# Performance work log

Measured on AMD Instinct MI355X. Metric: run time of the kernel, lower is better.

Reference implementation:

```python
import jax, jax.numpy as jnp
import numpy as np

N_NODES = 50000
N_EDGES = 800000
NEG_SLOPE = 0.2  # GATConv default
BN_EPS = 1e-5


def _seg_softmax(logits, seg, n):
    # per-target-node softmax over incoming edges (PyG softmax w/ +1e-16)
    m = jax.ops.segment_max(logits, seg, num_segments=n)
    m = jnp.where(jnp.isfinite(m), m, 0.0)
    e = jnp.exp(logits - m[seg])
    s = jax.ops.segment_sum(e, seg, num_segments=n)
    return e / (s[seg] + 1e-16)


def _gat_conv(x, src, dst, W, a_src, a_dst, b, concat):
    # x: [N, Fin]; W: [Fin, H*C]; a_src/a_dst: [H, C]
    n = x.shape[0]
    H, C = a_src.shape
    h = (x @ W).reshape(n, H, C)
    al_s = jnp.einsum('nhc,hc->nh', h, a_src)
    al_d = jnp.einsum('nhc,hc->nh', h, a_dst)
    logits = jax.nn.leaky_relu(al_s[src] + al_d[dst], NEG_SLOPE)  # [E, H]
    alpha = _seg_softmax(logits, dst, n)                           # [E, H]
    out = jax.ops.segment_sum(h[src] * alpha[:, :, None], dst, num_segments=n)
    out = out.reshape(n, H * C) if concat else out.mean(axis=1)
    return out + b


def _bn(x, g, b):
    mu = jnp.mean(x, axis=0)
    var = jnp.mean((x - mu) ** 2, axis=0)
    return (x - mu) * jax.lax.rsqrt(var + BN_EPS) * g + b


def _gat_params(key, fin, heads, ch, scale=0.1):
    k1, k2, k3 = jax.random.split(key, 3)
    W = jax.random.normal(k1, (fin, heads * ch), jnp.float32) * scale
    a_s = jax.random.normal(k2, (heads, ch), jnp.float32) * scale
    a_d = jax.random.normal(k3, (heads, ch), jnp.float32) * scale
    return W, a_s, a_d


def setup_inputs() -> dict:
    key = jax.random.key(0)
    ks = jax.random.split(key, 12)
    inp = {}
    inp['x'] = jax.random.normal(ks[0], (N_NODES, 3), jnp.float32)
    inp['edge_index'] = jax.random.randint(ks[1], (2, N_EDGES), 0, N_NODES, jnp.int64 if jax.config.jax_enable_x64 else jnp.int32)
    inp['W11'], inp['as11'], inp['ad11'] = _gat_params(ks[2], 3, 8, 8)
    inp['b11'] = jnp.zeros((64,), jnp.float32)
    inp['W12'], inp['as12'], inp['ad12'] = _gat_params(ks[3], 64, 8, 8)
    inp['b12'] = jnp.zeros((64,), jnp.float32)
    inp['g1'] = jnp.ones((64,), jnp.float32)
    inp['be1'] = jnp.zeros((64,), jnp.float32)
    inp['W21'], inp['as21'], inp['ad21'] = _gat_params(ks[4], 64, 8, 32)
    inp['b21'] = jnp.zeros((256,), jnp.float32)
    inp['W22'], inp['as22'], inp['ad22'] = _gat_params(ks[5], 256, 8, 32)
    inp['b22'] = jnp.zeros((256,), jnp.float32)
    inp['g2'] = jnp.ones((256,), jnp.float32)
    inp['be2'] = jnp.zeros((256,), jnp.float32)
    inp['W31'], inp['as31'], inp['ad31'] = _gat_params(ks[6], 256, 8, 64)
    inp['b31'] = jnp.zeros((512,), jnp.float32)
    inp['W32'], inp['as32'], inp['ad32'] = _gat_params(ks[7], 512, 8, 1)
    inp['b32'] = jnp.zeros((1,), jnp.float32)
    return inp


def reference(x, edge_index,
              W11, as11, ad11, b11, W12, as12, ad12, b12, g1, be1,
              W21, as21, ad21, b21, W22, as22, ad22, b22, g2, be2,
              W31, as31, ad31, b31, W32, as32, ad32, b32):
    n = x.shape[0]
    loops = jnp.arange(n, dtype=edge_index.dtype)
    src = jnp.concatenate([edge_index[0], loops])  # add_self_loops=True
    dst = jnp.concatenate([edge_index[1], loops])
    # GAT(3, 64, 2): conv -> relu -> conv
    h = jax.nn.relu(_gat_conv(x, src, dst, W11, as11, ad11, b11, True))
    h = _gat_conv(h, src, dst, W12, as12, ad12, b12, True)
    h = jax.nn.leaky_relu(_bn(h, g1, be1), 0.1)
    # GAT(64, 256, 2)
    h = jax.nn.relu(_gat_conv(h, src, dst, W21, as21, ad21, b21, True))
    h = _gat_conv(h, src, dst, W22, as22, ad22, b22, True)
    h = jax.nn.leaky_relu(_bn(h, g2, be2), 0.1)
    # GAT(256, 512, 2, 1): conv -> relu -> conv(concat=False)
    h = jax.nn.relu(_gat_conv(h, src, dst, W31, as31, ad31, b31, True))
    h = _gat_conv(h, src, dst, W32, as32, ad32, b32, False)
    return jax.nn.sigmoid(h)
```

## Files before the change

### kernel.cpp

```cpp
#include <hip/hip_runtime.h>
#include <math.h>

typedef short short8 __attribute__((ext_vector_type(8)));
typedef short short4v __attribute__((ext_vector_type(4)));
typedef float f32x4 __attribute__((ext_vector_type(4)));

__device__ __forceinline__ unsigned short f2bf(float v){
  unsigned u = __builtin_bit_cast(unsigned, v);
  u += 0x7FFFu + ((u >> 16) & 1u);
  return (unsigned short)(u >> 16);
}
__device__ __forceinline__ float bf2f(unsigned short b){
  unsigned u = ((unsigned)b) << 16;
  return __builtin_bit_cast(float, u);
}

__global__ void k_deg_prep(const int* __restrict__ dstv, int* __restrict__ deg, int E,
                           const float* __restrict__ W11, const float* __restrict__ W12,
                           const float* __restrict__ W21, const float* __restrict__ W22,
                           const float* __restrict__ W31,
                           unsigned short* __restrict__ bh, unsigned short* __restrict__ bl){
  int i = blockIdx.x*blockDim.x + threadIdx.x;
  if (i < E) atomicAdd(&deg[dstv[i]], 1);
  if (i < 221184){
    const float* W; int K, kpsh, off, Nn;
    if (i < 4096)       { W=W11; K=3;   kpsh=6; off=0;     Nn=64;  }
    else if (i < 8192)  { W=W12; K=64;  kpsh=6; off=4096;  Nn=64;  }
    else if (i < 24576) { W=W21; K=64;  kpsh=6; off=8192;  Nn=256; }
    else if (i < 90112) { W=W22; K=256; kpsh=8; off=24576; Nn=256; }
    else                { W=W31; K=256; kpsh=8; off=90112; Nn=512; }
    int j = i - off;
    int Kp = 1 << kpsh;
    int n = j >> kpsh, k = j & (Kp-1);
    float v = (k < K) ? W[(size_t)k*Nn + n] : 0.0f;
    unsigned short h = f2bf(v);
    bh[i] = h;
    bl[i] = f2bf(v - bf2f(h));
  }
}

__global__ __launch_bounds__(1024)
void k_scan1(const int* __restrict__ deg, int* __restrict__ off,
             int* __restrict__ bsum, int N){
  __shared__ int wpre[16];
  int tid = threadIdx.x;
  int lane = tid & 63, wv = tid >> 6;
  int i = blockIdx.x*1024 + tid;
  int v = (i < N) ? deg[i] : 0;
  int incl = v;
  #pragma unroll
  for (int d = 1; d < 64; d <<= 1){
    int t = __shfl_up(incl, d, 64);
    if (lane >= d) incl += t;
  }
  if (lane == 63) wpre[wv] = incl;
  __syncthreads();
  if (tid < 16){
    int x = wpre[tid];
    int ix = x;
    #pragma unroll
    for (int d = 1; d < 16; d <<= 1){
      int t = __shfl_up(ix, d, 16);
      if (tid >= d) ix += t;
    }
    wpre[tid] = ix - x;
    if (tid == 15) bsum[blockIdx.x] = ix;
  }
  __syncthreads();
  if (i < N) off[i+1] = wpre[wv] + incl;
}

__global__ void k_scan2(int* __restrict__ bsum, int* __restrict__ bpre, int nb){
  int t = threadIdx.x;
  int v = (t < nb) ? bsum[t] : 0;
  int incl = v;
  #pragma unroll
  for (int d = 1; d < 64; d <<= 1){
    int u = __shfl_up(incl, d, 64);
    if (t >= d) incl += u;
  }
  if (t < nb) bpre[t] = incl - v;
}

__global__ __launch_bounds__(1024)
void k_scan3(const int* __restrict__ deg, int* __restrict__ off,
             const int* __restrict__ bpre, int* __restrict__ cursor, int N){
  int i = blockIdx.x*1024 + threadIdx.x;
  if (i < N){
    int base = bpre[blockIdx.x];
    int incl = off[i+1] + base;
    off[i+1] = incl;
    cursor[i] = incl - deg[i];
    if (i == 0) off[0] = 0;
  }
}

__global__ void k_fill(const int* __restrict__ srcv, const int* __restrict__ dstv,
                       int* __restrict__ cursor, int* __restrict__ csr, int E){
  int e = blockIdx.x*blockDim.x + threadIdx.x;
  if (e < E){
    int d = dstv[e];
    int p = atomicAdd(&cursor[d], 1);
    csr[p] = srcv[e];
  }
}

__global__ __launch_bounds__(256)
void k_bn_stats(const unsigned short* __restrict__ x, float* __restrict__ psum,
                float* __restrict__ psq, int N, int HC){
  int f   = threadIdx.x & (HC-1);
  int sub = threadIdx.x / HC;
  int subs = 256 / HC;
  int slot = blockIdx.x*subs + sub;
  int stride = gridDim.x*subs;
  float s = 0.f, q = 0.f;
  for (int r = slot; r < N; r += stride){
    float v = bf2f(x[(size_t)r*HC + f]);
    s += v; q += v*v;
  }
  psum[(size_t)slot*HC + f] = s;
  psq [(size_t)slot*HC + f] = q;
}

__global__ __launch_bounds__(256)
void k_bn_coef(const float* __restrict__ psum, const float* __restrict__ psq,
               const float* __restrict__ g, const float* __restrict__ b,
               float* __restrict__ sc, float* __restrict__ sh,
               float invN, int HC, int nb){
  int f = blockIdx.x;
  int t = threadIdx.x;
  float s = 0.f, q = 0.f;
  for (int r = t; r < nb; r += 256){
    s += psum[(size_t)r*HC + f];
    q += psq [(size_t)r*HC + f];
  }
  #pragma unroll
  for (int d = 1; d < 64; d <<= 1){
    s += __shfl_xor(s, d, 64);
    q += __shfl_xor(q, d, 64);
  }
  __shared__ float ss[4], qq[4];
  int wv = t >> 6, ln = t & 63;
  if (ln == 0){ ss[wv] = s; qq[wv] = q; }
  __syncthreads();
  if (t == 0){
    s = ss[0]+ss[1]+ss[2]+ss[3];
    q = qq[0]+qq[1]+qq[2]+qq[3];
    float mu  = s*invN;
    float var = q*invN - mu*mu;
    float rs  = rsqrtf(var + 1e-5f) * g[f];
    sc[f] = rs;
    sh[f] = b[f] - mu*rs;
  }
}

template<int BN, int AFMT>
__global__ __launch_bounds__((BN==64)?256:512)
void gemm_mfma(const void* __restrict__ Av, const unsigned short* __restrict__ Bh,
               const unsigned short* __restrict__ Bl,
               const float* __restrict__ bnsc, const float* __restrict__ bnsh,
               const float* __restrict__ a_s, const float* __restrict__ a_d,
               unsigned short* __restrict__ Pb, float* __restrict__ Ds,
               float* __restrict__ Dd, int M, int K){
  constexpr int WAVES   = (BN==64) ? 4 : 8;
  constexpr int BLOCK   = WAVES*64;
  constexpr int WAVES_N = BN/64;
  constexpr int WAVES_M = WAVES/WAVES_N;
  constexpr int WM      = 64/WAVES_M;
  constexpr int MF      = WM/16;
  constexpr int CH      = (BN==512)?64 : (BN==256)?32 : 8;
  constexpr int TERMS   = (AFMT==0) ? 3 : 2;
  const int Kp = (K + 63) & ~(int)63;

  __shared__ char lds[(TERMS==3)?16384:8192];

  int tid  = threadIdx.x;
  int lane = tid & 63;
  int wid  = tid >> 6;
  int wn = wid % WAVES_N;
  int wm = wid / WAVES_N;
  int n0w = wn*64;
  int wm0 = wm*WM;
  int m0 = blockIdx.x * 64;

  f32x4 acc[MF][4];
  #pragma unroll
  for (int i = 0; i < MF; ++i)
    #pragma unroll
    for (int j = 0; j < 4; ++j)
      acc[i][j] = (f32x4){0.f,0.f,0.f,0.f};

  constexpr int SITER = 512/BLOCK;

  for (int k0 = 0; k0 < Kp; k0 += 64){
    __syncthreads();
    #pragma unroll
    for (int it = 0; it < SITER; ++it){
      int i = it*BLOCK + tid;
      int row = i >> 3, c8 = i & 7;
      int gm = m0 + row;
      int gk = k0 + c8*8;
      int off = row*128 + ((c8 ^ (row&7))<<4);
      if constexpr (AFMT == 2){
        short8 hv = {0,0,0,0,0,0,0,0};
        if (gm < M) hv = *(const short8*)((const unsigned short*)Av + (size_t)gm*K + gk);
        *(short8*)(lds + off) = hv;
      } else if constexpr (AFMT == 1){
        short8 raw = {0,0,0,0,0,0,0,0};
        if (gm < M) raw = *(const short8*)((const unsigned short*)Av + (size_t)gm*K + gk);
        short8 hi;
        #pragma unroll
        for (int j=0;j<8;++j){
          float u = bf2f((unsigned short)raw[j])*bnsc[gk+j] + bnsh[gk+j];
          u = u > 0.f ? u : 0.1f*u;
          if (gm >= M) u = 0.f;
          hi[j] = (short)f2bf(u);
        }
        *(short8*)(lds + off) = hi;
      } else {
        const float* A = (const float*)Av;
        float v[8];
        if (gm < M && gk + 8 <= K){
          const float* ap = A + (size_t)gm*K + gk;
          float4 x0 = *(const float4*)ap;
          float4 x1 = *(const float4*)(ap+4);
          v[0]=x0.x; v[1]=x0.y; v[2]=x0.z; v[3]=x0.w;
          v[4]=x1.x; v[5]=x1.y; v[6]=x1.z; v[7]=x1.w;
        } else {
          #pragma unroll
          for (int j=0;j<8;++j){
            int gkj = gk + j;
            v[j] = (gm < M && gkj < K) ? A[(size_t)gm*K + gkj] : 0.0f;
          }
        }
        short8 hi, lo;
        #pragma unroll
        for (int j=0;j<8;++j){
          unsigned short hb = f2bf(v[j]);
          hi[j] = (short)hb;
          lo[j] = (short)f2bf(v[j] - bf2f(hb));
        }
        *(short8*)(lds + off) = hi;
        *(short8*)(lds + 8192 + off) = lo;
      }
    }
    __syncthreads();
    #pragma unroll
    for (int kk = 0; kk < 2; ++kk){
      short8 bhf[4], blf[4];
      #pragma unroll
      for (int nf = 0; nf < 4; ++nf){
        int ncol = n0w + nf*16 + (lane & 15);
        int kidx = k0 + kk*32 + ((lane>>4)<<3);
        size_t bo = (size_t)ncol*Kp + kidx;
        bhf[nf] = *(const short8*)(Bh + bo);
        blf[nf] = *(const short8*)(Bl + bo);
      }
      #pragma unroll
      for (int mt = 0; mt < MF; ++mt){
        int row = wm0 + mt*16 + (lane & 15);
        int c8 = kk*4 + (lane>>4);
        int off = row*128 + ((c8 ^ (row&7))<<4);
        short8 ah = *(const short8*)(lds + off);
        #pragma unroll
        for (int nf = 0; nf < 4; ++nf){
          acc[mt][nf] = __builtin_amdgcn_mfma_f32_16x16x32_bf16(ah, bhf[nf], acc[mt][nf], 0,0,0);
          acc[mt][nf] = __builtin_amdgcn_mfma_f32_16x16x32_bf16(ah, blf[nf], acc[mt][nf], 0,0,0);
        }
        if constexpr (TERMS == 3){
          short8 al = *(const short8*)(lds + 8192 + off);
          #pragma unroll
          for (int nf = 0; nf < 4; ++nf)
            acc[mt][nf] = __builtin_amdgcn_mfma_f32_16x16x32_bf16(al, bhf[nf], acc[mt][nf], 0,0,0);
        }
      }
    }
  }

  float asv[4], adv[4];
  #pragma unroll
  for (int nf=0; nf<4; ++nf){
    int gcol = n0w + nf*16 + (lane&15);
    asv[nf] = a_s[gcol];
    adv[nf] = a_d[gcol];
  }
  #pragma unroll
  for (int mt = 0; mt < MF; ++mt){
    #pragma unroll
    for (int r = 0; r < 4; ++r){
      int gm = m0 + wm0 + mt*16 + ((lane>>4)<<2) + r;
      bool ok = gm < M;
      #pragma unroll
      for (int nf=0;nf<4;++nf){
        if (ok) Pb[(size_t)gm*BN + n0w + nf*16 + (lane&15)] = f2bf(acc[mt][nf][r]);
      }
      if constexpr (CH == 64){
        float ps = acc[mt][0][r]*asv[0] + acc[mt][1][r]*asv[1]
                 + acc[mt][2][r]*asv[2] + acc[mt][3][r]*asv[3];
        float pd = acc[mt][0][r]*adv[0] + acc[mt][1][r]*adv[1]
                 + acc[mt][2][r]*adv[2] + acc[mt][3][r]*adv[3];
        #pragma unroll
        for (int d2=1; d2<16; d2<<=1){ ps += __shfl_xor(ps,d2,64); pd += __shfl_xor(pd,d2,64); }
        if (ok && (lane&15)==0){
          int head = n0w >> 6;
          Ds[(size_t)gm*8 + head] = ps;
          Dd[(size_t)gm*8 + head] = pd;
        }
      } else if constexpr (CH == 32){
        float ps0 = acc[mt][0][r]*asv[0] + acc[mt][1][r]*asv[1];
        float ps1 = acc[mt][2][r]*asv[2] + acc[mt][3][r]*asv[3];
        float pd0 = acc[mt][0][r]*adv[0] + acc[mt][1][r]*adv[1];
        float pd1 = acc[mt][2][r]*adv[2] + acc[mt][3][r]*adv[3];
        #pragma unroll
        for (int d2=1; d2<16; d2<<=1){
          ps0 += __shfl_xor(ps0,d2,64); ps1 += __shfl_xor(ps1,d2,64);
          pd0 += __shfl_xor(pd0,d2,64); pd1 += __shfl_xor(pd1,d2,64);
        }
        if (ok && (lane&15)==0){
          int head = n0w >> 5;
          Ds[(size_t)gm*8 + head]     = ps0;
          Ds[(size_t)gm*8 + head + 1] = ps1;
          Dd[(size_t)gm*8 + head]     = pd0;
          Dd[(size_t)gm*8 + head + 1] = pd1;
        }
      } else {
        #pragma unroll
        for (int nf=0;nf<4;++nf){
          float ps = acc[mt][nf][r]*asv[nf];
          float pd = acc[mt][nf][r]*adv[nf];
          #pragma unroll
          for (int d2=1; d2<8; d2<<=1){ ps += __shfl_xor(ps,d2,64); pd += __shfl_xor(pd,d2,64); }
          if (ok && (lane&7)==0){
            int head = nf*2 + ((lane>>3)&1);
            Ds[(size_t)gm*8 + head] = ps;
            Dd[(size_t)gm*8 + head] = pd;
          }
        }
      }
    }
  }
}

template<int HC, int ACT>
__global__ __launch_bounds__(256)
void k_agg(const unsigned short* __restrict__ Pb, const float* __restrict__ Ds,
           const float* __restrict__ Dd, const int* __restrict__ off,
           const int* __restrict__ csr, const float* __restrict__ bias,
           unsigned short* __restrict__ outb, int N){
  __shared__ float salpha[4][512];
  int lane = threadIdx.x & 63;
  int wid  = threadIdx.x >> 6;
  int n = blockIdx.x*4 + wid;
  if (n >= N) return;
  int o0 = off[n], deg = off[n+1]-o0;

  float aldn[8];
  {
    const float* dn = Dd + (unsigned)n*8u;
    float4 x0 = *(const float4*)dn;
    float4 x1 = *(const float4*)(dn+4);
    aldn[0]=x0.x; aldn[1]=x0.y; aldn[2]=x0.z; aldn[3]=x0.w;
    aldn[4]=x1.x; aldn[5]=x1.y; aldn[6]=x1.z; aldn[7]=x1.w;
  }

  if (deg < 64){
    int nE = deg + 1;
    int myidx = (lane < deg) ? csr[o0+lane] : n;
    bool active = (lane < nE);
    float v[8];
    {
      const float* dp = Ds + (unsigned)myidx*8u;
      float4 x0 = *(const float4*)dp;
      float4 x1 = *(const float4*)(dp+4);
      float t[8] = {x0.x,x0.y,x0.z,x0.w,x1.x,x1.y,x1.z,x1.w};
      #pragma unroll
      for (int h=0;h<8;++h){
        float u = t[h] + aldn[h];
        u = u > 0.f ? u : 0.2f*u;
        v[h] = active ? u : -1e30f;
      }
    }
    float m[8];
    #pragma unroll
    for (int h=0;h<8;++h) m[h]=v[h];
    #pragma unroll
    for (int d=1; d<64; d<<=1)
      #pragma unroll
      for (int h=0;h<8;++h) m[h] = fmaxf(m[h], __shfl_xor(m[h], d, 64));
    float sv[8], s[8];
    #pragma unroll
    for (int h=0;h<8;++h){ sv[h] = active ? __expf(v[h]-m[h]) : 0.f; s[h]=sv[h]; }
    #pragma unroll
    for (int d=1; d<64; d<<=1)
      #pragma unroll
      for (int h=0;h<8;++h) s[h] += __shfl_xor(s[h], d, 64);
    if (active){
      #pragma unroll
      for (int h=0;h<8;++h) salpha[wid][lane*8+h] = sv[h] / (s[h] + 1e-16f);
    }
    asm volatile("s_waitcnt lgkmcnt(0)" ::: "memory");

    if constexpr (HC == 512){
      int myh = lane >> 3;
      float acc[8] = {0,0,0,0,0,0,0,0};
      const unsigned short* Pl = Pb + lane*8;
      for (int e=0; e<nE; ++e){
        int src = __shfl(myidx, e, 64);
        float alpha = salpha[wid][e*8 + myh];
        short8 w = *(const short8*)(Pl + (unsigned)src*512u);
        #pragma unroll
        for (int j=0;j<8;++j) acc[j] += alpha * bf2f((unsigned short)w[j]);
      }
      #pragma unroll
      for (int j=0;j<8;++j){
        int f = lane*8 + j;
        float u = acc[j] + bias[f];
        if (ACT == 1) u = fmaxf(u, 0.0f);
        outb[(unsigned)n*512u + f] = f2bf(u);
      }
    } else if constexpr (HC == 256){
      int sub = lane >> 5, fl = lane & 31;
      int h = fl >> 2;
      float acc[8] = {0,0,0,0,0,0,0,0};
      const unsigned short* Pl = Pb + fl*8;
      for (int e=0; e<nE; e+=2){
        int eg = e + sub;
        bool val = eg < nE;
        int src = __shfl(myidx, val ? eg : 0, 64);
        float alpha = val ? salpha[wid][eg*8 + h] : 0.f;
        short8 w = *(const short8*)(Pl + (unsigned)src*256u);
        #pragma unroll
        for (int j=0;j<8;++j) acc[j] += alpha * bf2f((unsigned short)w[j]);
      }
      #pragma unroll
      for (int j=0;j<8;++j) acc[j] += __shfl_xor(acc[j], 32, 64);
      if (sub == 0){
        short8 ov;
        #pragma unroll
        for (int j=0;j<8;++j){
          int f = fl*8 + j;
          float u = acc[j] + bias[f];
          if (ACT == 1) u = fmaxf(u, 0.0f);
          ov[j] = (short)f2bf(u);
        }
        *(short8*)(outb + (unsigned)n*256u + fl*8) = ov;
      }
    } else {
      int sub = lane >> 3, fl = lane & 7;
      float acc[8] = {0,0,0,0,0,0,0,0};
      const unsigned short* Pl = Pb + fl*8;
      for (int e=0; e<nE; e+=8){
        int eg = e + sub;
        bool val = eg < nE;
        int src = __shfl(myidx, val ? eg : 0, 64);
        float alpha = val ? salpha[wid][eg*8 + fl] : 0.f;
        short8 w = *(const short8*)(Pl + (unsigned)src*64u);
        #pragma unroll
        for (int j=0;j<8;++j) acc[j] += alpha * bf2f((unsigned short)w[j]);
      }
      #pragma unroll
      for (int j=0;j<8;++j){
        acc[j] += __shfl_xor(acc[j], 8, 64);
        acc[j] += __shfl_xor(acc[j], 16, 64);
        acc[j] += __shfl_xor(acc[j], 32, 64);
      }
      if (sub == 0){
        short8 ov;
        #pragma unroll
        for (int j=0;j<8;++j){
          int f = fl*8 + j;
          float u = acc[j] + bias[f];
          if (ACT == 1) u = fmaxf(u, 0.0f);
          ov[j] = (short)f2bf(u);
        }
        *(short8*)(outb + (unsigned)n*64u + fl*8) = ov;
      }
    }
  } else {
    constexpr int R = HC/64;
    int myh = lane >> 3;
    float m[8];
    #pragma unroll
    for (int h=0;h<8;++h) m[h] = -1e30f;
    for (int e = lane; e <= deg; e += 64){
      int src = (e < deg) ? csr[o0+e] : n;
      const float* ap = Ds + (size_t)src*8;
      #pragma unroll
      for (int h=0;h<8;++h){
        float u = ap[h] + aldn[h];
        u = u > 0.f ? u : 0.2f*u;
        m[h] = fmaxf(m[h], u);
      }
    }
    #pragma unroll
    for (int d=1; d<64; d<<=1)
      #pragma unroll
      for (int h=0;h<8;++h) m[h] = fmaxf(m[h], __shfl_xor(m[h], d, 64));
    float s[8] = {0,0,0,0,0,0,0,0};
    for (int e = lane; e <= deg; e += 64){
      int src = (e < deg) ? csr[o0+e] : n;
      const float* ap = Ds + (size_t)src*8;
      #pragma unroll
      for (int h=0;h<8;++h){
        float u = ap[h] + aldn[h];
        u = u > 0.f ? u : 0.2f*u;
        s[h] += __expf(u - m[h]);
      }
    }
    #pragma unroll
    for (int d=1; d<64; d<<=1)
      #pragma unroll
      for (int h=0;h<8;++h) s[h] += __shfl_xor(s[h], d, 64);
    float mh = m[myh];
    float rsh = 1.0f/(s[myh] + 1e-16f);
    float adh = aldn[myh];
    float acc[R];
    #pragma unroll
    for (int j=0;j<R;++j) acc[j]=0.f;
    for (int e = 0; e <= deg; ++e){
      int src = (e < deg) ? csr[o0+e] : n;
      float u = Ds[(size_t)src*8 + myh] + adh;
      u = u > 0.f ? u : 0.2f*u;
      float alpha = __expf(u - mh) * rsh;
      const unsigned short* hp = Pb + (size_t)src*HC + lane*R;
      if constexpr (R == 1){
        acc[0] += alpha * bf2f(hp[0]);
      } else if constexpr (R == 4){
        short4v w = *(const short4v*)hp;
        #pragma unroll
        for (int j=0;j<4;++j) acc[j] += alpha * bf2f((unsigned short)w[j]);
      } else {
        short8 w = *(const short8*)hp;
        #pragma unroll
        for (int j=0;j<8;++j) acc[j] += alpha * bf2f((unsigned short)w[j]);
      }
    }
    #pragma unroll
    for (int j = 0; j < R; ++j){
      int f = lane*R + j;
      float u = acc[j] + bias[f];
      if (ACT == 1) u = fmaxf(u, 0.0f);
      outb[(size_t)n*HC + f] = f2bf(u);
    }
  }
}

__global__ __launch_bounds__(256)
void gemm8(const unsigned short* __restrict__ Qb, const float* __restrict__ W,
           float* __restrict__ h8, int M){
  int lane = threadIdx.x & 63;
  int gw = (blockIdx.x*blockDim.x + threadIdx.x) >> 6;
  int nw = (gridDim.x*blockDim.x) >> 6;
  float w[8][8];
  const float* wp = W + lane*64;
  #pragma unroll
  for (int j=0;j<8;++j){
    float4 a = *(const float4*)(wp + j*8);
    float4 b = *(const float4*)(wp + j*8 + 4);
    w[j][0]=a.x; w[j][1]=a.y; w[j][2]=a.z; w[j][3]=a.w;
    w[j][4]=b.x; w[j][5]=b.y; w[j][6]=b.z; w[j][7]=b.w;
  }
  for (int n = gw; n < M; n += nw){
    short8 v8 = *(const short8*)(Qb + (size_t)n*512 + lane*8);
    float p[8] = {0,0,0,0,0,0,0,0};
    #pragma unroll
    for (int j=0;j<8;++j){
      float x = bf2f((unsigned short)v8[j]);
      #pragma unroll
      for (int o=0;o<8;++o) p[o] += x * w[j][o];
    }
    #pragma unroll
    for (int d=1; d<64; d<<=1)
      #pragma unroll
      for (int o=0;o<8;++o) p[o] += __shfl_xor(p[o], d, 64);
    if (lane == 0){
      float4 y0 = make_float4(p[0],p[1],p[2],p[3]);
      float4 y1 = make_float4(p[4],p[5],p[6],p[7]);
      *(float4*)(h8 + (size_t)n*8)     = y0;
      *(float4*)(h8 + (size_t)n*8 + 4) = y1;
    }
  }
}

__global__ __launch_bounds__(256)
void k_final(const float* __restrict__ h8, const float* __restrict__ a_s,
             const float* __restrict__ a_d, const int* __restrict__ off,
             const int* __restrict__ csr, const float* __restrict__ b32,
             float* __restrict__ outp, int N){
  int lane = threadIdx.x & 63;
  int wv   = threadIdx.x >> 6;
  int n = blockIdx.x*4 + wv;
  if (n >= N) return;
  int o0 = off[n], deg = off[n+1]-o0;
  float asv[8], adv[8];
  #pragma unroll
  for (int h=0;h<8;++h){ asv[h]=a_s[h]; adv[h]=a_d[h]; }
  float aldn[8];
  {
    const float* hp = h8 + (size_t)n*8;
    float4 x0 = *(const float4*)hp;
    float4 x1 = *(const float4*)(hp+4);
    float hn[8] = {x0.x,x0.y,x0.z,x0.w,x1.x,x1.y,x1.z,x1.w};
    #pragma unroll
    for (int h=0;h<8;++h) aldn[h] = hn[h]*adv[h];
  }

  if (deg < 64){
    int nE = deg + 1;
    int src = (lane < deg) ? csr[o0+lane] : n;
    bool act = (lane < nE);
    float hs[8];
    {
      const float* hp = h8 + (size_t)src*8;
      float4 x0 = *(const float4*)hp;
      float4 x1 = *(const float4*)(hp+4);
      hs[0]=x0.x; hs[1]=x0.y; hs[2]=x0.z; hs[3]=x0.w;
      hs[4]=x1.x; hs[5]=x1.y; hs[6]=x1.z; hs[7]=x1.w;
    }
    float v[8];
    #pragma unroll
    for (int h=0;h<8;++h){
      float u = hs[h]*asv[h] + aldn[h];
      u = u > 0.f ? u : 0.2f*u;
      v[h] = act ? u : -1e30f;
    }
    float m[8];
    #pragma unroll
    for (int h=0;h<8;++h) m[h]=v[h];
    #pragma unroll
    for (int d=1; d<64; d<<=1)
      #pragma unroll
      for (int h=0;h<8;++h) m[h] = fmaxf(m[h], __shfl_xor(m[h], d, 64));
    float s[8], t[8];
    #pragma unroll
    for (int h=0;h<8;++h){
      float e = act ? __expf(v[h]-m[h]) : 0.f;
      s[h]=e; t[h]=e*hs[h];
    }
    #pragma unroll
    for (int d=1; d<64; d<<=1)
      #pragma unroll
      for (int h=0;h<8;++h){
        s[h] += __shfl_xor(s[h], d, 64);
        t[h] += __shfl_xor(t[h], d, 64);
      }
    if (lane == 0){
      float o = 0.f;
      #pragma unroll
      for (int h=0;h<8;++h) o += t[h]/(s[h]+1e-16f);
      o = o*0.125f + b32[0];
      outp[n] = 1.0f/(1.0f + __expf(-o));
    }
  } else if (lane == 0){
    float m[8], s[8], agg[8];
    #pragma unroll
    for (int h=0;h<8;++h){ m[h]=-1e30f; s[h]=0.f; agg[h]=0.f; }
    for (int e = 0; e <= deg; ++e){
      int src = (e < deg) ? csr[o0+e] : n;
      #pragma unroll
      for (int h=0;h<8;++h){
        float u = h8[(size_t)src*8+h]*asv[h] + aldn[h];
        u = u > 0.f ? u : 0.2f*u;
        m[h] = fmaxf(m[h], u);
      }
    }
    for (int e = 0; e <= deg; ++e){
      int src = (e < deg) ? csr[o0+e] : n;
      #pragma unroll
      for (int h=0;h<8;++h){
        float u = h8[(size_t)src*8+h]*asv[h] + aldn[h];
        u = u > 0.f ? u : 0.2f*u;
        float ex = __expf(u - m[h]);
        s[h] += ex;
        agg[h] += ex * h8[(size_t)src*8+h];
      }
    }
    float o = 0.f;
    #pragma unroll
    for (int h=0;h<8;++h) o += agg[h]/(s[h]+1e-16f);
    o = o*0.125f + b32[0];
    outp[n] = 1.0f/(1.0f + __expf(-o));
  }
}

extern "C" void kernel_launch(void* const* d_in, const int* in_sizes, int n_in,
                              void* d_out, int out_size, void* d_ws, size_t ws_size,
                              hipStream_t stream){
  int N = in_sizes[0]/3;
  int E = in_sizes[1]/2;
  const float* x    = (const float*)d_in[0];
  const int*   ei   = (const int*)  d_in[1];
  const float* W11  = (const float*)d_in[2];
  const float* as11 = (const float*)d_in[3];
  const float* ad11 = (const float*)d_in[4];
  const float* b11  = (const float*)d_in[5];
  const float* W12  = (const float*)d_in[6];
  const float* as12 = (const float*)d_in[7];
  const float* ad12 = (const float*)d_in[8];
  const float* b12  = (const float*)d_in[9];
  const float* g1   = (const float*)d_in[10];
  const float* be1  = (const float*)d_in[11];
  const float* W21  = (const float*)d_in[12];
  const float* as21 = (const float*)d_in[13];
  const float* ad21 = (const float*)d_in[14];
  const float* b21  = (const float*)d_in[15];
  const float* W22  = (const float*)d_in[16];
  const float* as22 = (const float*)d_in[17];
  const float* ad22 = (const float*)d_in[18];
  const float* b22  = (const float*)d_in[19];
  const float* g2   = (const float*)d_in[20];
  const float* be2  = (const float*)d_in[21];
  const float* W31  = (const float*)d_in[22];
  const float* as31 = (const float*)d_in[23];
  const float* ad31 = (const float*)d_in[24];
  const float* b31  = (const float*)d_in[25];
  const float* W32  = (const float*)d_in[26];
  const float* as32 = (const float*)d_in[27];
  const float* ad32 = (const float*)d_in[28];
  const float* b32  = (const float*)d_in[29];

  char* ws = (char*)d_ws;
  size_t o = 0;
  auto alloc = [&](size_t bytes)->char*{
    char* p = ws + o;
    o = (o + bytes + 255) & ~(size_t)255;
    return p;
  };
  int*   deg    = (int*)  alloc((size_t)N*4);
  int*   off    = (int*)  alloc((size_t)(N+1)*4);
  int*   cursor = (int*)  alloc((size_t)N*4);
  int*   csr    = (int*)  alloc((size_t)E*4);
  int*   bsum   = (int*)  alloc(64*4);
  int*   bpre   = (int*)  alloc(64*4);
  unsigned short* bh = (unsigned short*)alloc(221184*2);
  unsigned short* bl = (unsigned short*)alloc(221184*2);
  float* h8     = (float*)alloc((size_t)N*8*4);
  float* psum   = (float*)alloc(1024*64*4);
  float* psq    = (float*)alloc(1024*64*4);
  float* bnsc   = (float*)alloc(1024);
  float* bnsh   = (float*)alloc(1024);
  unsigned short* Pb = (unsigned short*)alloc((size_t)N*512*2);
  unsigned short* Qb = (unsigned short*)alloc((size_t)N*512*2);
  float* Dsb    = (float*)alloc((size_t)N*8*4);
  float* Ddb    = (float*)alloc((size_t)N*8*4);
  (void)ws_size;

  const int BT11=0, BT12=4096, BT21=8192, BT22=24576, BT31=90112;

  hipMemsetAsync(deg, 0, (size_t)N*4, stream);
  int eb = (E+255)/256;
  int nb1k = (N+1023)/1024;
  k_deg_prep<<<eb, 256, 0, stream>>>(ei+E, deg, E, W11, W12, W21, W22, W31, bh, bl);
  k_scan1<<<nb1k, 1024, 0, stream>>>(deg, off, bsum, N);
  k_scan2<<<1, 64, 0, stream>>>(bsum, bpre, nb1k);
  k_scan3<<<nb1k, 1024, 0, stream>>>(deg, off, bpre, cursor, N);
  k_fill<<<eb, 256, 0, stream>>>(ei, ei+E, cursor, csr, E);

  int mb = (N+63)/64;
  int nb4 = (N+3)/4;
  float invN = 1.0f/(float)N;

  gemm_mfma<64,0><<<mb, 256, 0, stream>>>(x, bh+BT11, bl+BT11, nullptr, nullptr,
                                          as11, ad11, Pb, Dsb, Ddb, N, 3);
  k_agg<64,1><<<nb4, 256, 0, stream>>>(Pb, Dsb, Ddb, off, csr, b11, Qb, N);

  gemm_mfma<64,2><<<mb, 256, 0, stream>>>(Qb, bh+BT12, bl+BT12, nullptr, nullptr,
                                          as12, ad12, Pb, Dsb, Ddb, N, 64);
  k_agg<64,0><<<nb4, 256, 0, stream>>>(Pb, Dsb, Ddb, off, csr, b12, Qb, N);
  k_bn_stats<<<256, 256, 0, stream>>>(Qb, psum, psq, N, 64);
  k_bn_coef<<<64, 256, 0, stream>>>(psum, psq, g1, be1, bnsc, bnsh, invN, 64, 1024);

  gemm_mfma<256,1><<<mb, 512, 0, stream>>>(Qb, bh+BT21, bl+BT21, bnsc, bnsh,
                                           as21, ad21, Pb, Dsb, Ddb, N, 64);
  k_agg<256,1><<<nb4, 256, 0, stream>>>(Pb, Dsb, Ddb, off, csr, b21, Qb, N);

  gemm_mfma<256,2><<<mb, 512, 0, stream>>>(Qb, bh+BT22, bl+BT22, nullptr, nullptr,
                                           as22, ad22, Pb, Dsb, Ddb, N, 256);
  k_agg<256,0><<<nb4, 256, 0, stream>>>(Pb, Dsb, Ddb, off, csr, b22, Qb, N);
  k_bn_stats<<<256, 256, 0, stream>>>(Qb, psum, psq, N, 256);
  k_bn_coef<<<256, 256, 0, stream>>>(psum, psq, g2, be2, bnsc, bnsh, invN, 256, 256);

  gemm_mfma<512,1><<<mb, 512, 0, stream>>>(Qb, bh+BT31, bl+BT31, bnsc, bnsh,
                                           as31, ad31, Pb, Dsb, Ddb, N, 256);
  k_agg<512,1><<<nb4, 256, 0, stream>>>(Pb, Dsb, Ddb, off, csr, b31, Qb, N);

  gemm8<<<1024, 256, 0, stream>>>(Qb, W32, h8, N);
  k_final<<<nb4, 256, 0, stream>>>(h8, as32, ad32, off, csr, b32,
                                   (float*)d_out, N);
}
```

Before: 1.031 ms.

## Fuse batchnorm statistics and final 512x8 projection into aggregation kernels

The aggregation kernel gains a MODE template parameter. MODE 1 accumulates per-feature sum and sum-of-squares in shared memory with atomics and writes per-block partials, which removes the separate k_bn_stats pass that re-read the bf16 activations. MODE 2 multiplies each aggregated row by W32 held in shared memory and writes the 8-wide projection directly, which drops gemm8 and the 512-wide bf16 write and read of the last layer. In exchange, shared-memory atomic contention rises, and k_bn_coef now reduces over 12500 partial blocks instead of 256 or 1024.

After: 1.226 ms. 1.19x slower.

```diff
diff --git a/kernel.cpp b/kernel.cpp
--- a/kernel.cpp
+++ b/kernel.cpp
@@ -106,23 +106,6 @@
 }
 
 __global__ __launch_bounds__(256)
-void k_bn_stats(const unsigned short* __restrict__ x, float* __restrict__ psum,
-                float* __restrict__ psq, int N, int HC){
-  int f   = threadIdx.x & (HC-1);
-  int sub = threadIdx.x / HC;
-  int subs = 256 / HC;
-  int slot = blockIdx.x*subs + sub;
-  int stride = gridDim.x*subs;
-  float s = 0.f, q = 0.f;
-  for (int r = slot; r < N; r += stride){
-    float v = bf2f(x[(size_t)r*HC + f]);
-    s += v; q += v*v;
-  }
-  psum[(size_t)slot*HC + f] = s;
-  psq [(size_t)slot*HC + f] = q;
-}
-
-__global__ __launch_bounds__(256)
 void k_bn_coef(const float* __restrict__ psum, const float* __restrict__ psq,
                const float* __restrict__ g, const float* __restrict__ b,
                float* __restrict__ sc, float* __restrict__ sh,
@@ -341,243 +324,277 @@
   }
 }
 
-template<int HC, int ACT>
+template<int HC, int ACT, int MODE>
 __global__ __launch_bounds__(256)
 void k_agg(const unsigned short* __restrict__ Pb, const float* __restrict__ Ds,
            const float* __restrict__ Dd, const int* __restrict__ off,
            const int* __restrict__ csr, const float* __restrict__ bias,
-           unsigned short* __restrict__ outb, int N){
+           unsigned short* __restrict__ outb, float* __restrict__ x1,
+           float* __restrict__ x2, const float* __restrict__ W32, int N){
   __shared__ float salpha[4][512];
-  int lane = threadIdx.x & 63;
-  int wid  = threadIdx.x >> 6;
+  __shared__ float sstat[(MODE==1)? 2*HC : 1];
+  __shared__ float ws32[(MODE==2)? 4096 : 1];
+  int tid  = threadIdx.x;
+  int lane = tid & 63;
+  int wid  = tid >> 6;
+
+  if constexpr (MODE == 1){
+    if (tid < HC){ sstat[tid] = 0.f; sstat[HC+tid] = 0.f; }
+    __syncthreads();
+  }
+  if constexpr (MODE == 2){
+    #pragma unroll
+    for (int i = 0; i < 4; ++i){
+      float4 w4 = *(const float4*)(W32 + i*1024 + tid*4);
+      *(float4*)(ws32 + i*1024 + tid*4) = w4;
+    }
+    __syncthreads();
+  }
+
   int n = blockIdx.x*4 + wid;
-  if (n >= N) return;
-  int o0 = off[n], deg = off[n+1]-o0;
-
-  float aldn[8];
-  {
-    const float* dn = Dd + (unsigned)n*8u;
-    float4 x0 = *(const float4*)dn;
-    float4 x1 = *(const float4*)(dn+4);
-    aldn[0]=x0.x; aldn[1]=x0.y; aldn[2]=x0.z; aldn[3]=x0.w;
-    aldn[4]=x1.x; aldn[5]=x1.y; aldn[6]=x1.z; aldn[7]=x1.w;
-  }
-
-  if (deg < 64){
-    int nE = deg + 1;
-    int myidx = (lane < deg) ? csr[o0+lane] : n;
-    bool active = (lane < nE);
-    float v[8];
+  bool vn = (n < N);
+  float p8[8];
+  #pragma unroll
+  for (int o=0;o<8;++o) p8[o] = 0.f;
+
+  if (vn){
+    int o0 = off[n], deg = off[n+1]-o0;
+
+    float aldn[8];
     {
-      const float* dp = Ds + (unsigned)myidx*8u;
-      float4 x0 = *(const float4*)dp;
-      float4 x1 = *(const float4*)(dp+4);
-      float t[8] = {x0.x,x0.y,x0.z,x0.w,x1.x,x1.y,x1.z,x1.w};
-      #pragma unroll
-      for (int h=0;h<8;++h){
-        float u = t[h] + aldn[h];
+      const float* dn = Dd + (unsigned)n*8u;
+      float4 x0v = *(const float4*)dn;
+      float4 x1v = *(const float4*)(dn+4);
+      aldn[0]=x0v.x; aldn[1]=x0v.y; aldn[2]=x0v.z; aldn[3]=x0v.w;
+      aldn[4]=x1v.x; aldn[5]=x1v.y; aldn[6]=x1v.z; aldn[7]=x1v.w;
+    }
+
+    if (deg < 64){
+      int nE = deg + 1;
+      int myidx = (lane < deg) ? csr[o0+lane] : n;
+      bool active = (lane < nE);
+      float v[8];
+      {
+        const float* dp = Ds + (unsigned)myidx*8u;
+        float4 x0v = *(const float4*)dp;
+        float4 x1v = *(const float4*)(dp+4);
+        float t[8] = {x0v.x,x0v.y,x0v.z,x0v.w,x1v.x,x1v.y,x1v.z,x1v.w};
+        #pragma unroll
+        for (int h=0;h<8;++h){
+          float u = t[h] + aldn[h];
+          u = u > 0.f ? u : 0.2f*u;
+          v[h] = active ? u : -1e30f;
+        }
+      }
+      float m[8];
+      #pragma unroll
+      for (int h=0;h<8;++h) m[h]=v[h];
+      #pragma unroll
+      for (int d=1; d<64; d<<=1)
+        #pragma unroll
+        for (int h=0;h<8;++h) m[h] = fmaxf(m[h], __shfl_xor(m[h], d, 64));
+      float sv[8], s[8];
+      #pragma unroll
+      for (int h=0;h<8;++h){ sv[h] = active ? __expf(v[h]-m[h]) : 0.f; s[h]=sv[h]; }
+      #pragma unroll
+      for (int d=1; d<64; d<<=1)
+        #pragma unroll
+        for (int h=0;h<8;++h) s[h] += __shfl_xor(s[h], d, 64);
+      if (active){
+        #pragma unroll
+        for (int h=0;h<8;++h) salpha[wid][lane*8+h] = sv[h] / (s[h] + 1e-16f);
+      }
+      asm volatile("s_waitcnt lgkmcnt(0)" ::: "memory");
+
+      if constexpr (HC == 512){
+        int myh = lane >> 3;
+        float acc[8] = {0,0,0,0,0,0,0,0};
+        const unsigned short* Pl = Pb + lane*8;
+        for (int e=0; e<nE; ++e){
+          int src = __shfl(myidx, e, 64);
+          float alpha = salpha[wid][e*8 + myh];
+          short8 w = *(const short8*)(Pl + (unsigned)src*512u);
+          #pragma unroll
+          for (int j=0;j<8;++j) acc[j] += alpha * bf2f((unsigned short)w[j]);
+        }
+        #pragma unroll
+        for (int j=0;j<8;++j){
+          int f = lane*8 + j;
+          float u = acc[j] + bias[f];
+          if (ACT == 1) u = fmaxf(u, 0.0f);
+          if constexpr (MODE == 2){
+            #pragma unroll
+            for (int o=0;o<8;++o) p8[o] += u * ws32[f*8+o];
+          } else {
+            outb[(unsigned)n*512u + f] = f2bf(u);
+            if constexpr (MODE == 1){
+              atomicAdd(&sstat[f], u);
+              atomicAdd(&sstat[HC+f], u*u);
+            }
+          }
+        }
+      } else if constexpr (HC == 256){
+        int sub = lane >> 5, fl = lane & 31;
+        int h = fl >> 2;
+        float acc[8] = {0,0,0,0,0,0,0,0};
+        const unsigned short* Pl = Pb + fl*8;
+        for (int e=0; e<nE; e+=2){
+          int eg = e + sub;
+          bool val = eg < nE;
+          int src = __shfl(myidx, val ? eg : 0, 64);
+          float alpha = val ? salpha[wid][eg*8 + h] : 0.f;
+          short8 w = *(const short8*)(Pl + (unsigned)src*256u);
+          #pragma unroll
+          for (int j=0;j<8;++j) acc[j] += alpha * bf2f((unsigned short)w[j]);
+        }
+        #pragma unroll
+        for (int j=0;j<8;++j) acc[j] += __shfl_xor(acc[j], 32, 64);
+        if (sub == 0){
+          short8 ov;
+          #pragma unroll
+          for (int j=0;j<8;++j){
+            int f = fl*8 + j;
+            float u = acc[j] + bias[f];
+            if (ACT == 1) u = fmaxf(u, 0.0f);
+            ov[j] = (short)f2bf(u);
+            if constexpr (MODE == 1){
+              atomicAdd(&sstat[f], u);
+              atomicAdd(&sstat[HC+f], u*u);
+            }
+          }
+          *(short8*)(outb + (unsigned)n*256u + fl*8) = ov;
+        }
+      } else {
+        int sub = lane >> 3, fl = lane & 7;
+        float acc[8] = {0,0,0,0,0,0,0,0};
+        const unsigned short* Pl = Pb + fl*8;
+        for (int e=0; e<nE; e+=8){
+          int eg = e + sub;
+          bool val = eg < nE;
+          int src = __shfl(myidx, val ? eg : 0, 64);
+          float alpha = val ? salpha[wid][eg*8 + fl] : 0.f;
+          short8 w = *(const short8*)(Pl + (unsigned)src*64u);
+          #pragma unroll
+          for (int j=0;j<8;++j) acc[j] += alpha * bf2f((unsigned short)w[j]);
+        }
+        #pragma unroll
+        for (int j=0;j<8;++j){
+          acc[j] += __shfl_xor(acc[j], 8, 64);
+          acc[j] += __shfl_xor(acc[j], 16, 64);
+          acc[j] += __shfl_xor(acc[j], 32, 64);
+        }
+        if (sub == 0){
+          short8 ov;
+          #pragma unroll
+          for (int j=0;j<8;++j){
+            int f = fl*8 + j;
+            float u = acc[j] + bias[f];
+            if (ACT == 1) u = fmaxf(u, 0.0f);
+            ov[j] = (short)f2bf(u);
+            if constexpr (MODE == 1){
+              atomicAdd(&sstat[f], u);
+              atomicAdd(&sstat[HC+f], u*u);
+            }
+          }
+          *(short8*)(outb + (unsigned)n*64u + fl*8) = ov;
+        }
+      }
+    } else {
+      constexpr int R = HC/64;
+      int myh = lane >> 3;
+      float m[8];
+      #pragma unroll
+      for (int h=0;h<8;++h) m[h] = -1e30f;
+      for (int e = lane; e <= deg; e += 64){
+        int src = (e < deg) ? csr[o0+e] : n;
+        const float* ap = Ds + (size_t)src*8;
+        #pragma unroll
+        for (int h=0;h<8;++h){
+          float u = ap[h] + aldn[h];
+          u = u > 0.f ? u : 0.2f*u;
+          m[h] = fmaxf(m[h], u);
+        }
+      }
+      #pragma unroll
+      for (int d=1; d<64; d<<=1)
+        #pragma unroll
+        for (int h=0;h<8;++h) m[h] = fmaxf(m[h], __shfl_xor(m[h], d, 64));
+      float s[8] = {0,0,0,0,0,0,0,0};
+      for (int e = lane; e <= deg; e += 64){
+        int src = (e < deg) ? csr[o0+e] : n;
+        const float* ap = Ds + (size_t)src*8;
+        #pragma unroll
+        for (int h=0;h<8;++h){
+          float u = ap[h] + aldn[h];
+          u = u > 0.f ? u : 0.2f*u;
+          s[h] += __expf(u - m[h]);
+        }
+      }
+      #pragma unroll
+      for (int d=1; d<64; d<<=1)
+        #pragma unroll
+        for (int h=0;h<8;++h) s[h] += __shfl_xor(s[h], d, 64);
+      float mh = m[myh];
+      float rsh = 1.0f/(s[myh] + 1e-16f);
+      float adh = aldn[myh];
+      float acc[R];
+      #pragma unroll
+      for (int j=0;j<R;++j) acc[j]=0.f;
+      for (int e = 0; e <= deg; ++e){
+        int src = (e < deg) ? csr[o0+e] : n;
+        float u = Ds[(size_t)src*8 + myh] + adh;
         u = u > 0.f ? u : 0.2f*u;
-        v[h] = active ? u : -1e30f;
-      }
-    }
-    float m[8];
-    #pragma unroll
-    for (int h=0;h<8;++h) m[h]=v[h];
-    #pragma unroll
-    for (int d=1; d<64; d<<=1)
-      #pragma unroll
-      for (int h=0;h<8;++h) m[h] = fmaxf(m[h], __shfl_xor(m[h], d, 64));
-    float sv[8], s[8];
-    #pragma unroll
-    for (int h=0;h<8;++h){ sv[h] = active ? __expf(v[h]-m[h]) : 0.f; s[h]=sv[h]; }
-    #pragma unroll
-    for (int d=1; d<64; d<<=1)
-      #pragma unroll
-      for (int h=0;h<8;++h) s[h] += __shfl_xor(s[h], d, 64);
-    if (active){
-      #pragma unroll
-      for (int h=0;h<8;++h) salpha[wid][lane*8+h] = sv[h] / (s[h] + 1e-16f);
-    }
-    asm volatile("s_waitcnt lgkmcnt(0)" ::: "memory");
-
-    if constexpr (HC == 512){
-      int myh = lane >> 3;
-      float acc[8] = {0,0,0,0,0,0,0,0};
-      const unsigned short* Pl = Pb + lane*8;
-      for (int e=0; e<nE; ++e){
-        int src = __shfl(myidx, e, 64);
-        float alpha = salpha[wid][e*8 + myh];
-        short8 w = *(const short8*)(Pl + (unsigned)src*512u);
-        #pragma unroll
-        for (int j=0;j<8;++j) acc[j] += alpha * bf2f((unsigned short)w[j]);
-      }
-      #pragma unroll
-      for (int j=0;j<8;++j){
-        int f = lane*8 + j;
+        float alpha = __expf(u - mh) * rsh;
+        const unsigned short* hp = Pb + (size_t)src*HC + lane*R;
+        if constexpr (R == 1){
+          acc[0] += alpha * bf2f(hp[0]);
+        } else if constexpr (R == 4){
+          short4v w = *(const short4v*)hp;
+          #pragma unroll
+          for (int j=0;j<4;++j) acc[j] += alpha * bf2f((unsigned short)w[j]);
+        } else {
+          short8 w = *(const short8*)hp;
+          #pragma unroll
+          for (int j=0;j<8;++j) acc[j] += alpha * bf2f((unsigned short)w[j]);
+        }
+      }
+      #pragma unroll
+      for (int j = 0; j < R; ++j){
+        int f = lane*R + j;
         float u = acc[j] + bias[f];
         if (ACT == 1) u = fmaxf(u, 0.0f);
-        outb[(unsigned)n*512u + f] = f2bf(u);
-      }
-    } else if constexpr (HC == 256){
-      int sub = lane >> 5, fl = lane & 31;
-      int h = fl >> 2;
-      float acc[8] = {0,0,0,0,0,0,0,0};
-      const unsigned short* Pl = Pb + fl*8;
-      for (int e=0; e<nE; e+=2){
-        int eg = e + sub;
-        bool val = eg < nE;
-        int src = __shfl(myidx, val ? eg : 0, 64);
-        float alpha = val ? salpha[wid][eg*8 + h] : 0.f;
-        short8 w = *(const short8*)(Pl + (unsigned)src*256u);
-        #pragma unroll
-        for (int j=0;j<8;++j) acc[j] += alpha * bf2f((unsigned short)w[j]);
-      }
-      #pragma unroll
-      for (int j=0;j<8;++j) acc[j] += __shfl_xor(acc[j], 32, 64);
-      if (sub == 0){
-        short8 ov;
-        #pragma unroll
-        for (int j=0;j<8;++j){
-          int f = fl*8 + j;
-          float u = acc[j] + bias[f];
-          if (ACT == 1) u = fmaxf(u, 0.0f);
-          ov[j] = (short)f2bf(u);
-        }
-        *(short8*)(outb + (unsigned)n*256u + fl*8) = ov;
-      }
-    } else {
-      int sub = lane >> 3, fl = lane & 7;
-      float acc[8] = {0,0,0,0,0,0,0,0};
-      const unsigned short* Pl = Pb + fl*8;
-      for (int e=0; e<nE; e+=8){
-        int eg = e + sub;
-        bool val = eg < nE;
-        int src = __shfl(myidx, val ? eg : 0, 64);
-        float alpha = val ? salpha[wid][eg*8 + fl] : 0.f;
-        short8 w = *(const short8*)(Pl + (unsigned)src*64u);
-        #pragma unroll
-        for (int j=0;j<8;++j) acc[j] += alpha * bf2f((unsigned short)w[j]);
-      }
-      #pragma unroll
-      for (int j=0;j<8;++j){
-        acc[j] += __shfl_xor(acc[j], 8, 64);
-        acc[j] += __shfl_xor(acc[j], 16, 64);
-        acc[j] += __shfl_xor(acc[j], 32, 64);
-      }
-      if (sub == 0){
-        short8 ov;
-        #pragma unroll
-        for (int j=0;j<8;++j){
-          int f = fl*8 + j;
-          float u = acc[j] + bias[f];
-          if (ACT == 1) u = fmaxf(u, 0.0f);
-          ov[j] = (short)f2bf(u);
-        }
-        *(short8*)(outb + (unsigned)n*64u + fl*8) = ov;
-      }
-    }
-  } else {
-    constexpr int R = HC/64;
-    int myh = lane >> 3;
-    float m[8];
-    #pragma unroll
-    for (int h=0;h<8;++h) m[h] = -1e30f;
-    for (int e = lane; e <= deg; e += 64){
-      int src = (e < deg) ? csr[o0+e] : n;
-      const float* ap = Ds + (size_t)src*8;
-      #pragma unroll
-      for (int h=0;h<8;++h){
-        float u = ap[h] + aldn[h];
-        u = u > 0.f ? u : 0.2f*u;
-        m[h] = fmaxf(m[h], u);
-      }
-    }
-    #pragma unroll
-    for (int d=1; d<64; d<<=1)
-      #pragma unroll
-      for (int h=0;h<8;++h) m[h] = fmaxf(m[h], __shfl_xor(m[h], d, 64));
-    float s[8] = {0,0,0,0,0,0,0,0};
-    for (int e = lane; e <= deg; e += 64){
-      int src = (e < deg) ? csr[o0+e] : n;
-      const float* ap = Ds + (size_t)src*8;
-      #pragma unroll
-      for (int h=0;h<8;++h){
-        float u = ap[h] + aldn[h];
-        u = u > 0.f ? u : 0.2f*u;
-        s[h] += __expf(u - m[h]);
-      }
-    }
-    #pragma unroll
-    for (int d=1; d<64; d<<=1)
-      #pragma unroll
-      for (int h=0;h<8;++h) s[h] += __shfl_xor(s[h], d, 64);
-    float mh = m[myh];
-    float rsh = 1.0f/(s[myh] + 1e-16f);
-    float adh = aldn[myh];
-    float acc[R];
-    #pragma unroll
-    for (int j=0;j<R;++j) acc[j]=0.f;
-    for (int e = 0; e <= deg; ++e){
-      int src = (e < deg) ? csr[o0+e] : n;
-      float u = Ds[(size_t)src*8 + myh] + adh;
-      u = u > 0.f ? u : 0.2f*u;
-      float alpha = __expf(u - mh) * rsh;
-      const unsigned short* hp = Pb + (size_t)src*HC + lane*R;
-      if constexpr (R == 1){
-        acc[0] += alpha * bf2f(hp[0]);
-      } else if constexpr (R == 4){
-        short4v w = *(const short4v*)hp;
-        #pragma unroll
-        for (int j=0;j<4;++j) acc[j] += alpha * bf2f((unsigned short)w[j]);
-      } else {
-        short8 w = *(const short8*)hp;
-        #pragma unroll
-        for (int j=0;j<8;++j) acc[j] += alpha * bf2f((unsigned short)w[j]);
-      }
-    }
-    #pragma unroll
-    for (int j = 0; j < R; ++j){
-      int f = lane*R + j;
-      float u = acc[j] + bias[f];
-      if (ACT == 1) u = fmaxf(u, 0.0f);
-      outb[(size_t)n*HC + f] = f2bf(u);
-    }
-  }
-}
-
-__global__ __launch_bounds__(256)
-void gemm8(const unsigned short* __restrict__ Qb, const float* __restrict__ W,
-           float* __restrict__ h8, int M){
-  int lane = threadIdx.x & 63;
-  int gw = (blockIdx.x*blockDim.x + threadIdx.x) >> 6;
-  int nw = (gridDim.x*blockDim.x) >> 6;
-  float w[8][8];
-  const float* wp = W + lane*64;
-  #pragma unroll
-  for (int j=0;j<8;++j){
-    float4 a = *(const float4*)(wp + j*8);
-    float4 b = *(const float4*)(wp + j*8 + 4);
-    w[j][0]=a.x; w[j][1]=a.y; w[j][2]=a.z; w[j][3]=a.w;
-    w[j][4]=b.x; w[j][5]=b.y; w[j][6]=b.z; w[j][7]=b.w;
-  }
-  for (int n = gw; n < M; n += nw){
-    short8 v8 = *(const short8*)(Qb + (size_t)n*512 + lane*8);
-    float p[8] = {0,0,0,0,0,0,0,0};
-    #pragma unroll
-    for (int j=0;j<8;++j){
-      float x = bf2f((unsigned short)v8[j]);
-      #pragma unroll
-      for (int o=0;o<8;++o) p[o] += x * w[j][o];
-    }
-    #pragma unroll
-    for (int d=1; d<64; d<<=1)
-      #pragma unroll
-      for (int o=0;o<8;++o) p[o] += __shfl_xor(p[o], d, 64);
-    if (lane == 0){
-      float4 y0 = make_float4(p[0],p[1],p[2],p[3]);
-      float4 y1 = make_float4(p[4],p[5],p[6],p[7]);
-      *(float4*)(h8 + (size_t)n*8)     = y0;
-      *(float4*)(h8 + (size_t)n*8 + 4) = y1;
+        if constexpr (MODE == 2){
+          #pragma unroll
+          for (int o=0;o<8;++o) p8[o] += u * ws32[f*8+o];
+        } else {
+          outb[(size_t)n*HC + f] = f2bf(u);
+          if constexpr (MODE == 1){
+            atomicAdd(&sstat[f], u);
+            atomicAdd(&sstat[HC+f], u*u);
+          }
+        }
+      }
+    }
+
+    if constexpr (MODE == 2){
+      #pragma unroll
+      for (int d=1; d<64; d<<=1)
+        #pragma unroll
+        for (int o=0;o<8;++o) p8[o] += __shfl_xor(p8[o], d, 64);
+      if (lane == 0){
+        float4 y0 = make_float4(p8[0],p8[1],p8[2],p8[3]);
+        float4 y1 = make_float4(p8[4],p8[5],p8[6],p8[7]);
+        *(float4*)(x1 + (size_t)n*8)     = y0;
+        *(float4*)(x1 + (size_t)n*8 + 4) = y1;
+      }
+    }
+  }
+
+  if constexpr (MODE == 1){
+    __syncthreads();
+    if (tid < HC){
+      x1[(size_t)blockIdx.x*HC + tid] = sstat[tid];
+      x2[(size_t)blockIdx.x*HC + tid] = sstat[HC+tid];
     }
   }
 }
@@ -735,8 +752,9 @@
   unsigned short* bh = (unsigned short*)alloc(221184*2);
   unsigned short* bl = (unsigned short*)alloc(221184*2);
   float* h8     = (float*)alloc((size_t)N*8*4);
-  float* psum   = (float*)alloc(1024*64*4);
-  float* psq    = (float*)alloc(1024*64*4);
+  int nb4 = (N+3)/4;
+  float* psum   = (float*)alloc((size_t)nb4*256*4);
+  float* psq    = (float*)alloc((size_t)nb4*256*4);
   float* bnsc   = (float*)alloc(1024);
   float* bnsh   = (float*)alloc(1024);
   unsigned short* Pb = (unsigned short*)alloc((size_t)N*512*2);
@@ -757,34 +775,35 @@
   k_fill<<<eb, 256, 0, stream>>>(ei, ei+E, cursor, csr, E);
 
   int mb = (N+63)/64;
-  int nb4 = (N+3)/4;
   float invN = 1.0f/(float)N;
 
   gemm_mfma<64,0><<<mb, 256, 0, stream>>>(x, bh+BT11, bl+BT11, nullptr, nullptr,
                                           as11, ad11, Pb, Dsb, Ddb, N, 3);
-  k_agg<64,1><<<nb4, 256, 0, stream>>>(Pb, Dsb, Ddb, off, csr, b11, Qb, N);
+  k_agg<64,1,0><<<nb4, 256, 0, stream>>>(Pb, Dsb, Ddb, off, csr, b11, Qb,
+                                         nullptr, nullptr, nullptr, N);
 
   gemm_mfma<64,2><<<mb, 256, 0, stream>>>(Qb, bh+BT12, bl+BT12, nullptr, nullptr,
                                           as12, ad12, Pb, Dsb, Ddb, N, 64);
-  k_agg<64,0><<<nb4, 256, 0, stream>>>(Pb, Dsb, Ddb, off, csr, b12, Qb, N);
-  k_bn_stats<<<256, 256, 0, stream>>>(Qb, psum, psq, N, 64);
-  k_bn_coef<<<64, 256, 0, stream>>>(psum, psq, g1, be1, bnsc, bnsh, invN, 64, 1024);
+  k_agg<64,0,1><<<nb4, 256, 0, stream>>>(Pb, Dsb, Ddb, off, csr, b12, Qb,
+                                         psum, psq, nullptr, N);
+  k_bn_coef<<<64, 256, 0, stream>>>(psum, psq, g1, be1, bnsc, bnsh, invN, 64, nb4);
 
   gemm_mfma<256,1><<<mb, 512, 0, stream>>>(Qb, bh+BT21, bl+BT21, bnsc, bnsh,
                                            as21, ad21, Pb, Dsb, Ddb, N, 64);
-  k_agg<256,1><<<nb4, 256, 0, stream>>>(Pb, Dsb, Ddb, off, csr, b21, Qb, N);
+  k_agg<256,1,0><<<nb4, 256, 0, stream>>>(Pb, Dsb, Ddb, off, csr, b21, Qb,
+                                          nullptr, nullptr, nullptr, N);
 
   gemm_mfma<256,2><<<mb, 512, 0, stream>>>(Qb, bh+BT22, bl+BT22, nullptr, nullptr,
                                            as22, ad22, Pb, Dsb, Ddb, N, 256);
-  k_agg<256,0><<<nb4, 256, 0, stream>>>(Pb, Dsb, Ddb, off, csr, b22, Qb, N);
-  k_bn_stats<<<256, 256, 0, stream>>>(Qb, psum, psq, N, 256);
-  k_bn_coef<<<256, 256, 0, stream>>>(psum, psq, g2, be2, bnsc, bnsh, invN, 256, 256);
+  k_agg<256,0,1><<<nb4, 256, 0, stream>>>(Pb, Dsb, Ddb, off, csr, b22, Qb,
+                                          psum, psq, nullptr, N);
+  k_bn_coef<<<256, 256, 0, stream>>>(psum, psq, g2, be2, bnsc, bnsh, invN, 256, nb4);
 
   gemm_mfma<512,1><<<mb, 512, 0, stream>>>(Qb, bh+BT31, bl+BT31, bnsc, bnsh,
                                            as31, ad31, Pb, Dsb, Ddb, N, 256);
-  k_agg<512,1><<<nb4, 256, 0, stream>>>(Pb, Dsb, Ddb, off, csr, b31, Qb, N);
-
-  gemm8<<<1024, 256, 0, stream>>>(Qb, W32, h8, N);
+  k_agg<512,1,2><<<nb4, 256, 0, stream>>>(Pb, Dsb, Ddb, off, csr, b31, Qb,
+                                          h8, nullptr, W32, N);
+
   k_final<<<nb4, 256, 0, stream>>>(h8, as32, ad32, off, csr, b32,
                                    (float*)d_out, N);
 }
```
